# Kernel tuning notes

Hardware: AMD Instinct MI355X
Metric: run time of the kernel (lower is better)

Reference implementation:

```python
import jax, jax.numpy as jnp
import numpy as np

H = 128
N = 20000
E = 640000

def _lin_params(key, fan_in, fan_out, bias=True):
    k1, k2 = jax.random.split(key)
    bound = 1.0 / np.sqrt(fan_in)
    W = jax.random.uniform(k1, (fan_in, fan_out), jnp.float32, -bound, bound)
    if bias:
        b = jax.random.uniform(k2, (fan_out,), jnp.float32, -bound, bound)
        return W, b
    return W, None

def setup_inputs() -> dict:
    key = jax.random.key(0)
    ks = jax.random.split(key, 10)
    h = jax.random.normal(ks[0], (N, H), jnp.float32)
    pos = jax.random.normal(ks[1], (N, 3), jnp.float32)
    edge_index = jax.random.randint(ks[2], (2, E), 0, N, jnp.int64)
    eW1, eb1 = _lin_params(ks[3], 2 * H + 1, H)
    eW2, eb2 = _lin_params(ks[4], H, H)
    cW1, cb1 = _lin_params(ks[5], H, H)
    cW2, _ = _lin_params(ks[6], H, 1, bias=False)
    nW1, nb1 = _lin_params(ks[7], 2 * H, H)
    nW2, nb2 = _lin_params(ks[8], H, H)
    return {"h": h, "pos": pos, "edge_index": edge_index,
            "eW1": eW1, "eb1": eb1, "eW2": eW2, "eb2": eb2,
            "cW1": cW1, "cb1": cb1, "cW2": cW2,
            "nW1": nW1, "nb1": nb1, "nW2": nW2, "nb2": nb2}

def reference(h, pos, edge_index, eW1, eb1, eW2, eb2, cW1, cb1, cW2, nW1, nb1, nW2, nb2):
    row, col = edge_index[0], edge_index[1]
    n = h.shape[0]
    # per-edge geometry
    coord_diff = pos[row] - pos[col]                      # [E, 3]
    sq_dists = jnp.sum(coord_diff ** 2, axis=-1, keepdims=True)  # [E, 1]
    # edge MLP: Linear -> SiLU -> Linear -> SiLU
    edge_inputs = jnp.concatenate([h[row], h[col], sq_dists], axis=-1)  # [E, 2H+1]
    m_ij = jax.nn.silu(jax.nn.silu(edge_inputs @ eW1 + eb1) @ eW2 + eb2)  # [E, H]
    # coord MLP: Linear -> SiLU -> Linear(no bias) -> scalar weight per edge
    coord_weights = jax.nn.silu(m_ij @ cW1 + cb1) @ cW2   # [E, 1]
    norm_coord_diff = coord_diff / jnp.sqrt(sq_dists + 1e-8)
    pos_updates_ij = norm_coord_diff * coord_weights      # [E, 3]
    # scatter-mean over target nodes (zero where a node has no edges)
    pos_sum = jax.ops.segment_sum(pos_updates_ij, row, num_segments=n)
    cnt = jax.ops.segment_sum(jnp.ones((row.shape[0], 1), h.dtype), row, num_segments=n)
    pos_out = pos + pos_sum / jnp.maximum(cnt, 1.0)
    # scatter-add messages, then node MLP with residual
    m_i = jax.ops.segment_sum(m_ij, row, num_segments=n)  # [N, H]
    node_inputs = jnp.concatenate([h, m_i], axis=-1)      # [N, 2H]
    h_out = h + (jax.nn.silu(node_inputs @ nW1 + nb1) @ nW2 + nb2)
    return h_out, pos_out
```

## Files before the change

### kernel.cpp

```cpp
#include <hip/hip_runtime.h>
#include <hip/hip_bf16.h>
#include <cstdint>

#define H 128
#define NNODES 20000
#define NEDGES 640000
#define TILE 64
#define SCAN_BLOCKS 20

typedef unsigned short ushort_t;
typedef __attribute__((ext_vector_type(8))) short short8;
typedef __attribute__((ext_vector_type(4))) float floatx4;

__device__ __forceinline__ ushort_t f2bf(float f){
  uint32_t u = __builtin_bit_cast(uint32_t, f);
  u += 0x7fffu + ((u >> 16) & 1u);
  return (ushort_t)(u >> 16);
}
__device__ __forceinline__ float bf2f(ushort_t s){
  uint32_t u = ((uint32_t)s) << 16;
  return __builtin_bit_cast(float, u);
}
__device__ __forceinline__ uint32_t pk2bf(float lo, float hi){
  __hip_bfloat162 h2 = __float22bfloat162_rn(make_float2(lo, hi));
  uint32_t u;
  __builtin_memcpy(&u, &h2, 4);
  return u;
}
__device__ __forceinline__ float2 bfpair(uint32_t u){
  float2 r;
  uint32_t lo = u << 16, hi = u & 0xffff0000u;
  r.x = __builtin_bit_cast(float, lo);
  r.y = __builtin_bit_cast(float, hi);
  return r;
}
__device__ __forceinline__ float silu_f(float x){
  float e = __builtin_amdgcn_exp2f(-1.44269504089f * x);
  return x * __builtin_amdgcn_rcpf(1.f + e);
}

__global__ void setup_kernel(const float* __restrict__ eW1, const float* __restrict__ eW2,
                             const float* __restrict__ cW1, const float* __restrict__ nW1,
                             const float* __restrict__ nW2, const int* __restrict__ ei,
                             ushort_t* __restrict__ eW1t, ushort_t* __restrict__ eW2t,
                             ushort_t* __restrict__ cW1t, ushort_t* __restrict__ nW1t,
                             ushort_t* __restrict__ nW2t,
                             int* __restrict__ hist, float4* __restrict__ zbase){
  int idx = blockIdx.x * 256 + threadIdx.x;
  if (idx < 32768){
    int n = idx >> 8, k = idx & 255;
    eW1t[idx] = f2bf(eW1[k * H + n]);
  } else if (idx < 49152){
    int j = idx - 32768; int n = j >> 7, k = j & 127;
    eW2t[j] = f2bf(eW2[k * H + n]);
  } else if (idx < 65536){
    int j = idx - 49152; int n = j >> 7, k = j & 127;
    cW1t[j] = f2bf(cW1[k * H + n]);
  } else if (idx < 98304){
    int j = idx - 65536; int n = j >> 8, k = j & 255;
    nW1t[j] = f2bf(nW1[k * H + n]);
  } else if (idx < 114688){
    int j = idx - 98304; int n = j >> 7, k = j & 127;
    nW2t[j] = f2bf(nW2[k * H + n]);
  } else if (idx < 754688){
    int j = idx - 114688;
    atomicAdd(&hist[ei[j]], 1);
  } else {
    int j = idx - 754688;
    if (j < 655000) zbase[j] = make_float4(0.f, 0.f, 0.f, 0.f);
  }
}

__global__ void pq_kernel(const float* __restrict__ h, const ushort_t* __restrict__ eW1t,
                          ushort_t* __restrict__ Pb, ushort_t* __restrict__ Qb){
  const int t = threadIdx.x;
  const int lane = t & 63, q = lane >> 4, ln = lane & 15;
  const int nb = (t >> 6) * 32;
  const int c0 = nb + 2 * ln;
  const int base = blockIdx.x * 64;

  floatx4 accP[4][2], accQ[4][2];
  #pragma unroll
  for (int mt = 0; mt < 4; mt++)
    #pragma unroll
    for (int nt = 0; nt < 2; nt++){ accP[mt][nt] = (floatx4)0.f; accQ[mt][nt] = (floatx4)0.f; }

  #pragma unroll
  for (int ks = 0; ks < 4; ks++){
    short8 a[4];
    #pragma unroll
    for (int mt = 0; mt < 4; mt++){
      int node = base + mt*16 + ln;
      if (node >= NNODES) node = NNODES - 1;
      const float* hp = h + (size_t)node * H + ks*32 + q*8;
      float4 v0 = *(const float4*)hp;
      float4 v1 = *(const float4*)(hp + 4);
      uint32_t tw[4];
      tw[0] = pk2bf(v0.x, v0.y); tw[1] = pk2bf(v0.z, v0.w);
      tw[2] = pk2bf(v1.x, v1.y); tw[3] = pk2bf(v1.z, v1.w);
      __builtin_memcpy(&a[mt], tw, 16);
    }
    short8 bP[2], bQ[2];
    #pragma unroll
    for (int nt = 0; nt < 2; nt++){
      bP[nt] = *(const short8*)(eW1t + (size_t)(c0 + nt) * 256 + ks*32 + q*8);
      bQ[nt] = *(const short8*)(eW1t + (size_t)(c0 + nt) * 256 + 128 + ks*32 + q*8);
    }
    #pragma unroll
    for (int mt = 0; mt < 4; mt++)
      #pragma unroll
      for (int nt = 0; nt < 2; nt++){
        accP[mt][nt] = __builtin_amdgcn_mfma_f32_16x16x32_bf16(a[mt], bP[nt], accP[mt][nt], 0, 0, 0);
        accQ[mt][nt] = __builtin_amdgcn_mfma_f32_16x16x32_bf16(a[mt], bQ[nt], accQ[mt][nt], 0, 0, 0);
      }
  }
  #pragma unroll
  for (int mt = 0; mt < 4; mt++)
    #pragma unroll
    for (int r = 0; r < 4; r++){
      int node = base + mt*16 + q*4 + r;
      if (node < NNODES){
        *(uint32_t*)(Pb + (size_t)node * H + c0) = pk2bf(accP[mt][0][r], accP[mt][1][r]);
        *(uint32_t*)(Qb + (size_t)node * H + c0) = pk2bf(accQ[mt][0][r], accQ[mt][1][r]);
      }
    }
}

__global__ void scanA_kernel(const int* __restrict__ hist, int* __restrict__ head,
                             int* __restrict__ totals){
  __shared__ int s[1024];
  const int t = threadIdx.x;
  const int idx = blockIdx.x * 1024 + t;
  int v = (idx < NNODES) ? hist[idx] : 0;
  s[t] = v;
  __syncthreads();
  for (int off = 1; off < 1024; off <<= 1){
    int tmp = (t >= off) ? s[t - off] : 0;
    __syncthreads();
    s[t] += tmp;
    __syncthreads();
  }
  if (idx < NNODES) head[idx] = s[t] - v;
  if (t == 1023) totals[blockIdx.x] = s[t];
}

__global__ void scanC_kernel(const int* __restrict__ totals, int* __restrict__ head){
  __shared__ int off_s;
  if (threadIdx.x == 0){
    int a = 0;
    for (int i = 0; i < (int)blockIdx.x; i++) a += totals[i];
    off_s = a;
  }
  __syncthreads();
  int idx = blockIdx.x * 1024 + threadIdx.x;
  if (idx < NNODES) head[idx] += off_s;
}

__global__ void scatter_kernel(const int* __restrict__ ei, int* __restrict__ head,
                               int2* __restrict__ spair){
  int idx = blockIdx.x * 256 + threadIdx.x;
  if (idx < NEDGES){
    int r = ei[idx], c = ei[NEDGES + idx];
    int p = atomicAdd(&head[r], 1);
    spair[p] = make_int2(r, c);
  }
}

__global__ __launch_bounds__(256, 4) void edge_kernel(
    const ushort_t* __restrict__ Pb, const ushort_t* __restrict__ Qb,
    const float* __restrict__ pos, const int2* __restrict__ spair,
    const float* __restrict__ eW1, const float* __restrict__ eb1,
    const float* __restrict__ eb2, const float* __restrict__ cb1,
    const float* __restrict__ cW2,
    const ushort_t* __restrict__ eW2t, const ushort_t* __restrict__ cW1t,
    float* __restrict__ m_i, float* __restrict__ pos_sum)
{
  __shared__ __align__(16) ushort_t buf[TILE * 136];
  __shared__ int   row_l[TILE];
  __shared__ float sq_l[TILE];
  __shared__ float dx_l[TILE], dy_l[TILE], dz_l[TILE], w_l[TILE];

  const int t = threadIdx.x;
  const int base = blockIdx.x * TILE;
  const int lane = t & 63, q = lane >> 4, ln = lane & 15;
  const int nb = (t >> 6) * 32;
  const int c0 = nb + 2 * ln;

  if (t < TILE){
    int2 rc = spair[base + t];
    row_l[t] = rc.x;
    float ax = pos[rc.x*3+0] - pos[rc.y*3+0];
    float ay = pos[rc.x*3+1] - pos[rc.y*3+1];
    float az = pos[rc.x*3+2] - pos[rc.y*3+2];
    dx_l[t] = ax; dy_l[t] = ay; dz_l[t] = az;
    sq_l[t] = ax*ax + ay*ay + az*az;
    w_l[t]  = 0.f;
  }

  {
    const int i = t >> 2, p = t & 3;
    int2 rc = spair[base + i];
    float ax = pos[rc.x*3+0] - pos[rc.y*3+0];
    float ay = pos[rc.x*3+1] - pos[rc.y*3+1];
    float az = pos[rc.x*3+2] - pos[rc.y*3+2];
    float sq = ax*ax + ay*ay + az*az;
    const uint4*  Pp = (const uint4*)(Pb + (size_t)rc.x * H + p*32);
    const uint4*  Qp = (const uint4*)(Qb + (size_t)rc.y * H + p*32);
    const float4* wp = (const float4*)(eW1 + 256 * H + p*32);
    const float4* ep = (const float4*)(eb1 + p*32);
    ushort_t* dst = buf + i * 136 + p*32;
    #pragma unroll
    for (int j = 0; j < 4; j++){
      uint4 pv = Pp[j], qv = Qp[j];
      float4 w0 = wp[2*j], w1 = wp[2*j+1];
      float4 e0 = ep[2*j], e1 = ep[2*j+1];
      float2 p0 = bfpair(pv.x), p1 = bfpair(pv.y), p2 = bfpair(pv.z), p3 = bfpair(pv.w);
      float2 q0 = bfpair(qv.x), q1 = bfpair(qv.y), q2 = bfpair(qv.z), q3 = bfpair(qv.w);
      float f0 = p0.x + q0.x + sq * w0.x + e0.x;
      float f1 = p0.y + q0.y + sq * w0.y + e0.y;
      float f2 = p1.x + q1.x + sq * w0.z + e0.z;
      float f3 = p1.y + q1.y + sq * w0.w + e0.w;
      float f4 = p2.x + q2.x + sq * w1.x + e1.x;
      float f5 = p2.y + q2.y + sq * w1.y + e1.y;
      float f6 = p3.x + q3.x + sq * w1.z + e1.z;
      float f7 = p3.y + q3.y + sq * w1.w + e1.w;
      uint4 out;
      out.x = pk2bf(silu_f(f0), silu_f(f1));
      out.y = pk2bf(silu_f(f2), silu_f(f3));
      out.z = pk2bf(silu_f(f4), silu_f(f5));
      out.w = pk2bf(silu_f(f6), silu_f(f7));
      *(uint4*)(dst + j*8) = out;
    }
  }
  __syncthreads();

  floatx4 acc[4][2];

  #pragma unroll
  for (int mt = 0; mt < 4; mt++)
    #pragma unroll
    for (int nt = 0; nt < 2; nt++) acc[mt][nt] = (floatx4)0.f;
  #pragma unroll
  for (int ks = 0; ks < 4; ks++){
    short8 a[4], b[2];
    #pragma unroll
    for (int mt = 0; mt < 4; mt++)
      a[mt] = *(const short8*)(buf + (mt*16 + ln) * 136 + ks*32 + q*8);
    #pragma unroll
    for (int nt = 0; nt < 2; nt++)
      b[nt] = *(const short8*)(eW2t + (size_t)(c0 + nt) * 128 + ks*32 + q*8);
    #pragma unroll
    for (int mt = 0; mt < 4; mt++)
      #pragma unroll
      for (int nt = 0; nt < 2; nt++)
        acc[mt][nt] = __builtin_amdgcn_mfma_f32_16x16x32_bf16(a[mt], b[nt], acc[mt][nt], 0, 0, 0);
  }
  __syncthreads();
  {
    float2 e2 = *(const float2*)(eb2 + c0);
    #pragma unroll
    for (int mt = 0; mt < 4; mt++)
      #pragma unroll
      for (int r = 0; r < 4; r++){
        int m = mt*16 + q*4 + r;
        float f0 = silu_f(acc[mt][0][r] + e2.x);
        float f1 = silu_f(acc[mt][1][r] + e2.y);
        *(uint32_t*)(buf + m * 136 + c0) = pk2bf(f0, f1);
      }
  }
  __syncthreads();

  #pragma unroll
  for (int mt = 0; mt < 4; mt++)
    #pragma unroll
    for (int nt = 0; nt < 2; nt++) acc[mt][nt] = (floatx4)0.f;
  #pragma unroll
  for (int ks = 0; ks < 4; ks++){
    short8 a[4], b[2];
    #pragma unroll
    for (int mt = 0; mt < 4; mt++)
      a[mt] = *(const short8*)(buf + (mt*16 + ln) * 136 + ks*32 + q*8);
    #pragma unroll
    for (int nt = 0; nt < 2; nt++)
      b[nt] = *(const short8*)(cW1t + (size_t)(c0 + nt) * 128 + ks*32 + q*8);
    #pragma unroll
    for (int mt = 0; mt < 4; mt++)
      #pragma unroll
      for (int nt = 0; nt < 2; nt++)
        acc[mt][nt] = __builtin_amdgcn_mfma_f32_16x16x32_bf16(a[mt], b[nt], acc[mt][nt], 0, 0, 0);
  }
  {
    float2 c1 = *(const float2*)(cb1 + c0);
    float2 c2 = *(const float2*)(cW2 + c0);
    #pragma unroll
    for (int mt = 0; mt < 4; mt++)
      #pragma unroll
      for (int r = 0; r < 4; r++){
        float p = silu_f(acc[mt][0][r] + c1.x) * c2.x
                + silu_f(acc[mt][1][r] + c1.y) * c2.y;
        p += __shfl_xor(p, 1);
        p += __shfl_xor(p, 2);
        p += __shfl_xor(p, 4);
        p += __shfl_xor(p, 8);
        if (ln == 0) atomicAdd(&w_l[mt*16 + q*4 + r], p);
      }
  }
  __syncthreads();

  {
    int col = t & 127;
    int ms  = (t >> 7) * 32;
    float a0 = 0.f;
    int cur = row_l[ms];
    #pragma unroll 4
    for (int mm = 0; mm < 32; mm++){
      int m = ms + mm;
      int rr = row_l[m];
      float v = bf2f(buf[m * 136 + col]);
      if (rr != cur){
        unsafeAtomicAdd(&m_i[(size_t)cur * H + col], a0);
        a0 = 0.f; cur = rr;
      }
      a0 += v;
    }
    unsafeAtomicAdd(&m_i[(size_t)cur * H + col], a0);
  }
  if (t < 3){
    const float* src = (t == 0) ? dx_l : (t == 1) ? dy_l : dz_l;
    float accv = 0.f;
    int cur = row_l[0];
    for (int m = 0; m < TILE; m++){
      int rr = row_l[m];
      if (rr != cur){
        unsafeAtomicAdd(&pos_sum[cur*3 + t], accv);
        accv = 0.f; cur = rr;
      }
      float s = __builtin_amdgcn_rsqf(sq_l[m] + 1e-8f) * w_l[m];
      accv += src[m] * s;
    }
    unsafeAtomicAdd(&pos_sum[cur*3 + t], accv);
  }
}

__global__ __launch_bounds__(256, 3) void node_kernel(
    const float* __restrict__ h, const float* __restrict__ pos,
    const float* __restrict__ nb1, const float* __restrict__ nb2,
    const ushort_t* __restrict__ nW1t, const ushort_t* __restrict__ nW2t,
    const float* __restrict__ m_i, const float* __restrict__ pos_sum,
    const int* __restrict__ hist,
    float* __restrict__ h_out, float* __restrict__ pos_out)
{
  __shared__ __align__(16) ushort_t bufA[TILE * 264];
  __shared__ __align__(16) ushort_t bufT[TILE * 136];
  const int t = threadIdx.x;
  const int base = blockIdx.x * TILE;

  if (t < TILE){
    int node = base + t;
    if (node < NNODES){
      float c = fmaxf((float)hist[node], 1.f);
      float invc = __builtin_amdgcn_rcpf(c);
      pos_out[node*3+0] = pos[node*3+0] + pos_sum[node*3+0] * invc;
      pos_out[node*3+1] = pos[node*3+1] + pos_sum[node*3+1] * invc;
      pos_out[node*3+2] = pos[node*3+2] + pos_sum[node*3+2] * invc;
    }
  }
  {
    const int i = t >> 2, p = t & 3;
    const int node = base + i;
    ushort_t* dst = bufA + i * 264 + p * 64;
    if (node < NNODES){
      const float* s = (p < 2) ? (h + (size_t)node * H + p * 64)
                               : (m_i + (size_t)node * H + (p - 2) * 64);
      const float4* sp = (const float4*)s;
      #pragma unroll
      for (int j = 0; j < 8; j++){
        float4 v0 = sp[j*2], v1 = sp[j*2+1];
        uint4 uu;
        uu.x = pk2bf(v0.x, v0.y); uu.y = pk2bf(v0.z, v0.w);
        uu.z = pk2bf(v1.x, v1.y); uu.w = pk2bf(v1.z, v1.w);
        *(uint4*)(dst + j*8) = uu;
      }
    } else {
      #pragma unroll
      for (int j = 0; j < 8; j++) ((short8*)dst)[j] = (short8)0;
    }
  }
  __syncthreads();

  const int lane = t & 63, q = lane >> 4, ln = lane & 15;
  const int nb_ = (t >> 6) * 32;
  const int c0 = nb_ + 2 * ln;

  floatx4 acc[4][2];
  #pragma unroll
  for (int mt = 0; mt < 4; mt++)
    #pragma unroll
    for (int nt = 0; nt < 2; nt++) acc[mt][nt] = (floatx4)0.f;
  #pragma unroll
  for (int ks = 0; ks < 8; ks++){
    short8 a[4], b[2];
    #pragma unroll
    for (int mt = 0; mt < 4; mt++)
      a[mt] = *(const short8*)(bufA + (mt*16 + ln) * 264 + ks*32 + q*8);
    #pragma unroll
    for (int nt = 0; nt < 2; nt++)
      b[nt] = *(const short8*)(nW1t + (size_t)(c0 + nt) * 256 + ks*32 + q*8);
    #pragma unroll
    for (int mt = 0; mt < 4; mt++)
      #pragma unroll
      for (int nt = 0; nt < 2; nt++)
        acc[mt][nt] = __builtin_amdgcn_mfma_f32_16x16x32_bf16(a[mt], b[nt], acc[mt][nt], 0, 0, 0);
  }
  {
    float2 b1 = *(const float2*)(nb1 + c0);
    #pragma unroll
    for (int mt = 0; mt < 4; mt++)
      #pragma unroll
      for (int r = 0; r < 4; r++){
        int m = mt*16 + q*4 + r;
        float f0 = silu_f(acc[mt][0][r] + b1.x);
        float f1 = silu_f(acc[mt][1][r] + b1.y);
        *(uint32_t*)(bufT + m * 136 + c0) = pk2bf(f0, f1);
      }
  }
  __syncthreads();

  #pragma unroll
  for (int mt = 0; mt < 4; mt++)
    #pragma unroll
    for (int nt = 0; nt < 2; nt++) acc[mt][nt] = (floatx4)0.f;
  #pragma unroll
  for (int ks = 0; ks < 4; ks++){
    short8 a[4], b[2];
    #pragma unroll
    for (int mt = 0; mt < 4; mt++)
      a[mt] = *(const short8*)(bufT + (mt*16 + ln) * 136 + ks*32 + q*8);
    #pragma unroll
    for (int nt = 0; nt < 2; nt++)
      b[nt] = *(const short8*)(nW2t + (size_t)(c0 + nt) * 128 + ks*32 + q*8);
    #pragma unroll
    for (int mt = 0; mt < 4; mt++)
      #pragma unroll
      for (int nt = 0; nt < 2; nt++)
        acc[mt][nt] = __builtin_amdgcn_mfma_f32_16x16x32_bf16(a[mt], b[nt], acc[mt][nt], 0, 0, 0);
  }
  {
    float2 b2 = *(const float2*)(nb2 + c0);
    #pragma unroll
    for (int mt = 0; mt < 4; mt++)
      #pragma unroll
      for (int r = 0; r < 4; r++){
        int m = mt*16 + q*4 + r;
        int node = base + m;
        if (node < NNODES){
          const float2 hv = *(const float2*)(h + (size_t)node * H + c0);
          float2 o;
          o.x = hv.x + acc[mt][0][r] + b2.x;
          o.y = hv.y + acc[mt][1][r] + b2.y;
          *(float2*)(h_out + (size_t)node * H + c0) = o;
        }
      }
  }
}

extern "C" void kernel_launch(void* const* d_in, const int* in_sizes, int n_in,
                              void* d_out, int out_size, void* d_ws, size_t ws_size,
                              hipStream_t stream){
  const float* h   = (const float*)d_in[0];
  const float* pos = (const float*)d_in[1];
  const int*   ei  = (const int*)d_in[2];
  const float* eW1 = (const float*)d_in[3];
  const float* eb1 = (const float*)d_in[4];
  const float* eW2 = (const float*)d_in[5];
  const float* eb2 = (const float*)d_in[6];
  const float* cW1 = (const float*)d_in[7];
  const float* cb1 = (const float*)d_in[8];
  const float* cW2 = (const float*)d_in[9];
  const float* nW1 = (const float*)d_in[10];
  const float* nb1 = (const float*)d_in[11];
  const float* nW2 = (const float*)d_in[12];
  const float* nb2 = (const float*)d_in[13];

  char* ws = (char*)d_ws;
  float*    m_i     = (float*)   (ws);
  float*    pos_sum = (float*)   (ws + 10240000);
  int*      hist    = (int*)     (ws + 10480000);
  int*      head    = (int*)     (ws + 10560000);
  int*      totals  = (int*)     (ws + 10640000);
  int2*     spair   = (int2*)    (ws + 10644096);
  ushort_t* Pb      = (ushort_t*)(ws + 15764096);
  ushort_t* eW1t    = (ushort_t*)(ws + 20884096);
  ushort_t* eW2t    = (ushort_t*)(ws + 20949632);
  ushort_t* cW1t    = (ushort_t*)(ws + 20982400);
  ushort_t* nW1t    = (ushort_t*)(ws + 21015168);
  ushort_t* nW2t    = (ushort_t*)(ws + 21080704);
  ushort_t* Qb      = (ushort_t*)(ws + 21113472);

  (void)hipMemsetAsync(hist, 0, 80000, stream);

  setup_kernel<<<5507, 256, 0, stream>>>(eW1, eW2, cW1, nW1, nW2, ei,
                                         eW1t, eW2t, cW1t, nW1t, nW2t, hist,
                                         (float4*)ws);
  pq_kernel<<<(NNODES + 63) / 64, 256, 0, stream>>>(h, eW1t, Pb, Qb);
  scanA_kernel<<<SCAN_BLOCKS, 1024, 0, stream>>>(hist, head, totals);
  scanC_kernel<<<SCAN_BLOCKS, 1024, 0, stream>>>(totals, head);
  scatter_kernel<<<(NEDGES + 255) / 256, 256, 0, stream>>>(ei, head, spair);

  edge_kernel<<<NEDGES / TILE, 256, 0, stream>>>(Pb, Qb, pos, spair,
                                                 eW1, eb1, eb2, cb1, cW2,
                                                 eW2t, cW1t, m_i, pos_sum);

  float* h_out   = (float*)d_out;
  float* pos_out = h_out + (size_t)NNODES * H;
  node_kernel<<<(NNODES + TILE - 1) / TILE, 256, 0, stream>>>(h, pos, nb1, nb2,
                                                              nW1t, nW2t, m_i, pos_sum,
                                                              hist, h_out, pos_out);
}
```

Measured before the change: 404.6 us.

## Precompute h@nW1 in pq kernel and shrink node kernel tile to 32

Adds a third GEMM to pq_kernel computing h times the first half of nW1 into a bf16 buffer Rb. The node kernel then only multiplies m_i by the second half, reads m_i directly into registers, and uses 32-node tiles with less shared memory. Edge-kernel launch bounds are raised to 8, its first-layer elementwise math is packed into float2 ops, and its segment reduction handles two columns per thread. Rb adds a bf16 rounding of the partial sum and extra memory traffic, and the higher occupancy target may cause register spills.

```diff
diff --git a/kernel.cpp b/kernel.cpp
--- a/kernel.cpp
+++ b/kernel.cpp
@@ -11,15 +11,12 @@
 typedef unsigned short ushort_t;
 typedef __attribute__((ext_vector_type(8))) short short8;
 typedef __attribute__((ext_vector_type(4))) float floatx4;
+typedef __attribute__((ext_vector_type(2))) float floatx2;
 
 __device__ __forceinline__ ushort_t f2bf(float f){
   uint32_t u = __builtin_bit_cast(uint32_t, f);
   u += 0x7fffu + ((u >> 16) & 1u);
   return (ushort_t)(u >> 16);
-}
-__device__ __forceinline__ float bf2f(ushort_t s){
-  uint32_t u = ((uint32_t)s) << 16;
-  return __builtin_bit_cast(float, u);
 }
 __device__ __forceinline__ uint32_t pk2bf(float lo, float hi){
   __hip_bfloat162 h2 = __float22bfloat162_rn(make_float2(lo, hi));
@@ -27,11 +24,10 @@
   __builtin_memcpy(&u, &h2, 4);
   return u;
 }
-__device__ __forceinline__ float2 bfpair(uint32_t u){
-  float2 r;
-  uint32_t lo = u << 16, hi = u & 0xffff0000u;
-  r.x = __builtin_bit_cast(float, lo);
-  r.y = __builtin_bit_cast(float, hi);
+__device__ __forceinline__ floatx2 bfpair2(uint32_t u){
+  floatx2 r;
+  r.x = __builtin_bit_cast(float, u << 16);
+  r.y = __builtin_bit_cast(float, u & 0xffff0000u);
   return r;
 }
 __device__ __forceinline__ float silu_f(float x){
@@ -72,18 +68,22 @@
 }
 
 __global__ void pq_kernel(const float* __restrict__ h, const ushort_t* __restrict__ eW1t,
-                          ushort_t* __restrict__ Pb, ushort_t* __restrict__ Qb){
+                          const ushort_t* __restrict__ nW1t,
+                          ushort_t* __restrict__ Pb, ushort_t* __restrict__ Qb,
+                          ushort_t* __restrict__ Rb){
   const int t = threadIdx.x;
   const int lane = t & 63, q = lane >> 4, ln = lane & 15;
   const int nb = (t >> 6) * 32;
   const int c0 = nb + 2 * ln;
   const int base = blockIdx.x * 64;
 
-  floatx4 accP[4][2], accQ[4][2];
+  floatx4 accP[4][2], accQ[4][2], accR[4][2];
   #pragma unroll
   for (int mt = 0; mt < 4; mt++)
     #pragma unroll
-    for (int nt = 0; nt < 2; nt++){ accP[mt][nt] = (floatx4)0.f; accQ[mt][nt] = (floatx4)0.f; }
+    for (int nt = 0; nt < 2; nt++){
+      accP[mt][nt] = (floatx4)0.f; accQ[mt][nt] = (floatx4)0.f; accR[mt][nt] = (floatx4)0.f;
+    }
 
   #pragma unroll
   for (int ks = 0; ks < 4; ks++){
@@ -100,11 +100,12 @@
       tw[2] = pk2bf(v1.x, v1.y); tw[3] = pk2bf(v1.z, v1.w);
       __builtin_memcpy(&a[mt], tw, 16);
     }
-    short8 bP[2], bQ[2];
+    short8 bP[2], bQ[2], bR[2];
     #pragma unroll
     for (int nt = 0; nt < 2; nt++){
       bP[nt] = *(const short8*)(eW1t + (size_t)(c0 + nt) * 256 + ks*32 + q*8);
       bQ[nt] = *(const short8*)(eW1t + (size_t)(c0 + nt) * 256 + 128 + ks*32 + q*8);
+      bR[nt] = *(const short8*)(nW1t + (size_t)(c0 + nt) * 256 + ks*32 + q*8);
     }
     #pragma unroll
     for (int mt = 0; mt < 4; mt++)
@@ -112,6 +113,7 @@
       for (int nt = 0; nt < 2; nt++){
         accP[mt][nt] = __builtin_amdgcn_mfma_f32_16x16x32_bf16(a[mt], bP[nt], accP[mt][nt], 0, 0, 0);
         accQ[mt][nt] = __builtin_amdgcn_mfma_f32_16x16x32_bf16(a[mt], bQ[nt], accQ[mt][nt], 0, 0, 0);
+        accR[mt][nt] = __builtin_amdgcn_mfma_f32_16x16x32_bf16(a[mt], bR[nt], accR[mt][nt], 0, 0, 0);
       }
   }
   #pragma unroll
@@ -122,6 +124,7 @@
       if (node < NNODES){
         *(uint32_t*)(Pb + (size_t)node * H + c0) = pk2bf(accP[mt][0][r], accP[mt][1][r]);
         *(uint32_t*)(Qb + (size_t)node * H + c0) = pk2bf(accQ[mt][0][r], accQ[mt][1][r]);
+        *(uint32_t*)(Rb + (size_t)node * H + c0) = pk2bf(accR[mt][0][r], accR[mt][1][r]);
       }
     }
 }
@@ -166,7 +169,7 @@
   }
 }
 
-__global__ __launch_bounds__(256, 4) void edge_kernel(
+__global__ __launch_bounds__(256, 8) void edge_kernel(
     const ushort_t* __restrict__ Pb, const ushort_t* __restrict__ Qb,
     const float* __restrict__ pos, const int2* __restrict__ spair,
     const float* __restrict__ eW1, const float* __restrict__ eb1,
@@ -204,31 +207,25 @@
     float ay = pos[rc.x*3+1] - pos[rc.y*3+1];
     float az = pos[rc.x*3+2] - pos[rc.y*3+2];
     float sq = ax*ax + ay*ay + az*az;
-    const uint4*  Pp = (const uint4*)(Pb + (size_t)rc.x * H + p*32);
-    const uint4*  Qp = (const uint4*)(Qb + (size_t)rc.y * H + p*32);
-    const float4* wp = (const float4*)(eW1 + 256 * H + p*32);
-    const float4* ep = (const float4*)(eb1 + p*32);
+    floatx2 sq2; sq2.x = sq; sq2.y = sq;
+    const uint4*   Pp = (const uint4*)(Pb + (size_t)rc.x * H + p*32);
+    const uint4*   Qp = (const uint4*)(Qb + (size_t)rc.y * H + p*32);
+    const floatx2* wp = (const floatx2*)(eW1 + 256 * H + p*32);
+    const floatx2* ep = (const floatx2*)(eb1 + p*32);
     ushort_t* dst = buf + i * 136 + p*32;
     #pragma unroll
     for (int j = 0; j < 4; j++){
       uint4 pv = Pp[j], qv = Qp[j];
-      float4 w0 = wp[2*j], w1 = wp[2*j+1];
-      float4 e0 = ep[2*j], e1 = ep[2*j+1];
-      float2 p0 = bfpair(pv.x), p1 = bfpair(pv.y), p2 = bfpair(pv.z), p3 = bfpair(pv.w);
-      float2 q0 = bfpair(qv.x), q1 = bfpair(qv.y), q2 = bfpair(qv.z), q3 = bfpair(qv.w);
-      float f0 = p0.x + q0.x + sq * w0.x + e0.x;
-      float f1 = p0.y + q0.y + sq * w0.y + e0.y;
-      float f2 = p1.x + q1.x + sq * w0.z + e0.z;
-      float f3 = p1.y + q1.y + sq * w0.w + e0.w;
-      float f4 = p2.x + q2.x + sq * w1.x + e1.x;
-      float f5 = p2.y + q2.y + sq * w1.y + e1.y;
-      float f6 = p3.x + q3.x + sq * w1.z + e1.z;
-      float f7 = p3.y + q3.y + sq * w1.w + e1.w;
-      uint4 out;
-      out.x = pk2bf(silu_f(f0), silu_f(f1));
-      out.y = pk2bf(silu_f(f2), silu_f(f3));
-      out.z = pk2bf(silu_f(f4), silu_f(f5));
-      out.w = pk2bf(silu_f(f6), silu_f(f7));
+      uint32_t pvv[4] = {pv.x, pv.y, pv.z, pv.w};
+      uint32_t qvv[4] = {qv.x, qv.y, qv.z, qv.w};
+      uint32_t outv[4];
+      #pragma unroll
+      for (int e = 0; e < 4; e++){
+        floatx2 f = bfpair2(pvv[e]) + bfpair2(qvv[e]) + ep[j*4 + e];
+        f = f + sq2 * wp[j*4 + e];
+        outv[e] = pk2bf(silu_f(f.x), silu_f(f.y));
+      }
+      uint4 out; __builtin_memcpy(&out, outv, 16);
       *(uint4*)(dst + j*8) = out;
     }
   }
@@ -308,22 +305,25 @@
   __syncthreads();
 
   {
-    int col = t & 127;
-    int ms  = (t >> 7) * 32;
-    float a0 = 0.f;
+    int cp = (t & 63) * 2;
+    int ms = (t >> 6) * 16;
+    float a0 = 0.f, a1 = 0.f;
     int cur = row_l[ms];
     #pragma unroll 4
-    for (int mm = 0; mm < 32; mm++){
+    for (int mm = 0; mm < 16; mm++){
       int m = ms + mm;
       int rr = row_l[m];
-      float v = bf2f(buf[m * 136 + col]);
+      uint32_t v = *(const uint32_t*)(buf + m * 136 + cp);
       if (rr != cur){
-        unsafeAtomicAdd(&m_i[(size_t)cur * H + col], a0);
-        a0 = 0.f; cur = rr;
-      }
-      a0 += v;
-    }
-    unsafeAtomicAdd(&m_i[(size_t)cur * H + col], a0);
+        unsafeAtomicAdd(&m_i[(size_t)cur * H + cp],     a0);
+        unsafeAtomicAdd(&m_i[(size_t)cur * H + cp + 1], a1);
+        a0 = 0.f; a1 = 0.f; cur = rr;
+      }
+      floatx2 f = bfpair2(v);
+      a0 += f.x; a1 += f.y;
+    }
+    unsafeAtomicAdd(&m_i[(size_t)cur * H + cp],     a0);
+    unsafeAtomicAdd(&m_i[(size_t)cur * H + cp + 1], a1);
   }
   if (t < 3){
     const float* src = (t == 0) ? dx_l : (t == 1) ? dy_l : dz_l;
@@ -342,72 +342,54 @@
   }
 }
 
-__global__ __launch_bounds__(256, 3) void node_kernel(
+__global__ __launch_bounds__(256, 8) void node_kernel(
     const float* __restrict__ h, const float* __restrict__ pos,
     const float* __restrict__ nb1, const float* __restrict__ nb2,
     const ushort_t* __restrict__ nW1t, const ushort_t* __restrict__ nW2t,
+    const ushort_t* __restrict__ Rb,
     const float* __restrict__ m_i, const float* __restrict__ pos_sum,
     const int* __restrict__ hist,
     float* __restrict__ h_out, float* __restrict__ pos_out)
 {
-  __shared__ __align__(16) ushort_t bufA[TILE * 264];
-  __shared__ __align__(16) ushort_t bufT[TILE * 136];
+  __shared__ __align__(16) ushort_t bufT[32 * 136];
   const int t = threadIdx.x;
-  const int base = blockIdx.x * TILE;
-
-  if (t < TILE){
-    int node = base + t;
-    if (node < NNODES){
-      float c = fmaxf((float)hist[node], 1.f);
-      float invc = __builtin_amdgcn_rcpf(c);
-      pos_out[node*3+0] = pos[node*3+0] + pos_sum[node*3+0] * invc;
-      pos_out[node*3+1] = pos[node*3+1] + pos_sum[node*3+1] * invc;
-      pos_out[node*3+2] = pos[node*3+2] + pos_sum[node*3+2] * invc;
-    }
-  }
-  {
-    const int i = t >> 2, p = t & 3;
-    const int node = base + i;
-    ushort_t* dst = bufA + i * 264 + p * 64;
-    if (node < NNODES){
-      const float* s = (p < 2) ? (h + (size_t)node * H + p * 64)
-                               : (m_i + (size_t)node * H + (p - 2) * 64);
-      const float4* sp = (const float4*)s;
-      #pragma unroll
-      for (int j = 0; j < 8; j++){
-        float4 v0 = sp[j*2], v1 = sp[j*2+1];
-        uint4 uu;
-        uu.x = pk2bf(v0.x, v0.y); uu.y = pk2bf(v0.z, v0.w);
-        uu.z = pk2bf(v1.x, v1.y); uu.w = pk2bf(v1.z, v1.w);
-        *(uint4*)(dst + j*8) = uu;
-      }
-    } else {
-      #pragma unroll
-      for (int j = 0; j < 8; j++) ((short8*)dst)[j] = (short8)0;
-    }
-  }
-  __syncthreads();
-
+  const int base = blockIdx.x * 32;
   const int lane = t & 63, q = lane >> 4, ln = lane & 15;
   const int nb_ = (t >> 6) * 32;
   const int c0 = nb_ + 2 * ln;
 
-  floatx4 acc[4][2];
-  #pragma unroll
-  for (int mt = 0; mt < 4; mt++)
+  if (t < 32){
+    int node = base + t;
+    float c = fmaxf((float)hist[node], 1.f);
+    float invc = __builtin_amdgcn_rcpf(c);
+    pos_out[node*3+0] = pos[node*3+0] + pos_sum[node*3+0] * invc;
+    pos_out[node*3+1] = pos[node*3+1] + pos_sum[node*3+1] * invc;
+    pos_out[node*3+2] = pos[node*3+2] + pos_sum[node*3+2] * invc;
+  }
+
+  floatx4 acc[2][2];
+  #pragma unroll
+  for (int mt = 0; mt < 2; mt++)
     #pragma unroll
     for (int nt = 0; nt < 2; nt++) acc[mt][nt] = (floatx4)0.f;
   #pragma unroll
-  for (int ks = 0; ks < 8; ks++){
-    short8 a[4], b[2];
-    #pragma unroll
-    for (int mt = 0; mt < 4; mt++)
-      a[mt] = *(const short8*)(bufA + (mt*16 + ln) * 264 + ks*32 + q*8);
+  for (int ks = 0; ks < 4; ks++){
+    short8 a[2], b[2];
+    #pragma unroll
+    for (int mt = 0; mt < 2; mt++){
+      const float* mp = m_i + (size_t)(base + mt*16 + ln) * H + ks*32 + q*8;
+      float4 v0 = *(const float4*)mp;
+      float4 v1 = *(const float4*)(mp + 4);
+      uint32_t tw[4];
+      tw[0] = pk2bf(v0.x, v0.y); tw[1] = pk2bf(v0.z, v0.w);
+      tw[2] = pk2bf(v1.x, v1.y); tw[3] = pk2bf(v1.z, v1.w);
+      __builtin_memcpy(&a[mt], tw, 16);
+    }
     #pragma unroll
     for (int nt = 0; nt < 2; nt++)
-      b[nt] = *(const short8*)(nW1t + (size_t)(c0 + nt) * 256 + ks*32 + q*8);
-    #pragma unroll
-    for (int mt = 0; mt < 4; mt++)
+      b[nt] = *(const short8*)(nW1t + (size_t)(c0 + nt) * 256 + 128 + ks*32 + q*8);
+    #pragma unroll
+    for (int mt = 0; mt < 2; mt++)
       #pragma unroll
       for (int nt = 0; nt < 2; nt++)
         acc[mt][nt] = __builtin_amdgcn_mfma_f32_16x16x32_bf16(a[mt], b[nt], acc[mt][nt], 0, 0, 0);
@@ -415,51 +397,50 @@
   {
     float2 b1 = *(const float2*)(nb1 + c0);
     #pragma unroll
-    for (int mt = 0; mt < 4; mt++)
-      #pragma unroll
-      for (int r = 0; r < 4; r++){
-        int m = mt*16 + q*4 + r;
-        float f0 = silu_f(acc[mt][0][r] + b1.x);
-        float f1 = silu_f(acc[mt][1][r] + b1.y);
-        *(uint32_t*)(bufT + m * 136 + c0) = pk2bf(f0, f1);
-      }
-  }
-  __syncthreads();
-
-  #pragma unroll
-  for (int mt = 0; mt < 4; mt++)
-    #pragma unroll
-    for (int nt = 0; nt < 2; nt++) acc[mt][nt] = (floatx4)0.f;
-  #pragma unroll
-  for (int ks = 0; ks < 4; ks++){
-    short8 a[4], b[2];
-    #pragma unroll
-    for (int mt = 0; mt < 4; mt++)
-      a[mt] = *(const short8*)(bufT + (mt*16 + ln) * 136 + ks*32 + q*8);
-    #pragma unroll
-    for (int nt = 0; nt < 2; nt++)
-      b[nt] = *(const short8*)(nW2t + (size_t)(c0 + nt) * 128 + ks*32 + q*8);
-    #pragma unroll
-    for (int mt = 0; mt < 4; mt++)
-      #pragma unroll
-      for (int nt = 0; nt < 2; nt++)
-        acc[mt][nt] = __builtin_amdgcn_mfma_f32_16x16x32_bf16(a[mt], b[nt], acc[mt][nt], 0, 0, 0);
-  }
-  {
-    float2 b2 = *(const float2*)(nb2 + c0);
-    #pragma unroll
-    for (int mt = 0; mt < 4; mt++)
+    for (int mt = 0; mt < 2; mt++)
       #pragma unroll
       for (int r = 0; r < 4; r++){
         int m = mt*16 + q*4 + r;
         int node = base + m;
-        if (node < NNODES){
-          const float2 hv = *(const float2*)(h + (size_t)node * H + c0);
-          float2 o;
-          o.x = hv.x + acc[mt][0][r] + b2.x;
-          o.y = hv.y + acc[mt][1][r] + b2.y;
-          *(float2*)(h_out + (size_t)node * H + c0) = o;
-        }
+        floatx2 rf = bfpair2(*(const uint32_t*)(Rb + (size_t)node * H + c0));
+        float f0 = silu_f(acc[mt][0][r] + rf.x + b1.x);
+        float f1 = silu_f(acc[mt][1][r] + rf.y + b1.y);
+        *(uint32_t*)(bufT + m * 136 + c0) = pk2bf(f0, f1);
+      }
+  }
+  __syncthreads();
+
+  #pragma unroll
+  for (int mt = 0; mt < 2; mt++)
+    #pragma unroll
+    for (int nt = 0; nt < 2; nt++) acc[mt][nt] = (floatx4)0.f;
+  #pragma unroll
+  for (int ks = 0; ks < 4; ks++){
+    short8 a[2], b[2];
+    #pragma unroll
+    for (int mt = 0; mt < 2; mt++)
+      a[mt] = *(const short8*)(bufT + (mt*16 + ln) * 136 + ks*32 + q*8);
+    #pragma unroll
+    for (int nt = 0; nt < 2; nt++)
+      b[nt] = *(const short8*)(nW2t + (size_t)(c0 + nt) * 128 + ks*32 + q*8);
+    #pragma unroll
+    for (int mt = 0; mt < 2; mt++)
+      #pragma unroll
+      for (int nt = 0; nt < 2; nt++)
+        acc[mt][nt] = __builtin_amdgcn_mfma_f32_16x16x32_bf16(a[mt], b[nt], acc[mt][nt], 0, 0, 0);
+  }
+  {
+    float2 b2 = *(const float2*)(nb2 + c0);
+    #pragma unroll
+    for (int mt = 0; mt < 2; mt++)
+      #pragma unroll
+      for (int r = 0; r < 4; r++){
+        int node = base + mt*16 + q*4 + r;
+        const float2 hv = *(const float2*)(h + (size_t)node * H + c0);
+        float2 o;
+        o.x = hv.x + acc[mt][0][r] + b2.x;
+        o.y = hv.y + acc[mt][1][r] + b2.y;
+        *(float2*)(h_out + (size_t)node * H + c0) = o;
       }
   }
 }
@@ -496,13 +477,14 @@
   ushort_t* nW1t    = (ushort_t*)(ws + 21015168);
   ushort_t* nW2t    = (ushort_t*)(ws + 21080704);
   ushort_t* Qb      = (ushort_t*)(ws + 21113472);
+  ushort_t* Rb      = (ushort_t*)(ws + 26233472);
 
   (void)hipMemsetAsync(hist, 0, 80000, stream);
 
   setup_kernel<<<5507, 256, 0, stream>>>(eW1, eW2, cW1, nW1, nW2, ei,
                                          eW1t, eW2t, cW1t, nW1t, nW2t, hist,
                                          (float4*)ws);
-  pq_kernel<<<(NNODES + 63) / 64, 256, 0, stream>>>(h, eW1t, Pb, Qb);
+  pq_kernel<<<(NNODES + 63) / 64, 256, 0, stream>>>(h, eW1t, nW1t, Pb, Qb, Rb);
   scanA_kernel<<<SCAN_BLOCKS, 1024, 0, stream>>>(hist, head, totals);
   scanC_kernel<<<SCAN_BLOCKS, 1024, 0, stream>>>(totals, head);
   scatter_kernel<<<(NEDGES + 255) / 256, 256, 0, stream>>>(ei, head, spair);
@@ -513,7 +495,7 @@
 
   float* h_out   = (float*)d_out;
   float* pos_out = h_out + (size_t)NNODES * H;
-  node_kernel<<<(NNODES + TILE - 1) / TILE, 256, 0, stream>>>(h, pos, nb1, nb2,
-                                                              nW1t, nW2t, m_i, pos_sum,
-                                                              hist, h_out, pos_out);
-}
+  node_kernel<<<NNODES / 32, 256, 0, stream>>>(h, pos, nb1, nb2,
+                                               nW1t, nW2t, Rb, m_i, pos_sum,
+                                               hist, h_out, pos_out);
+}
```

New measurement: 416.4 us. +2.9%, slower.
